# Kernel tuning notes

Measured on AMD Instinct MI355X. Metric: run time of the kernel, lower is better.

The kernel has to match this reference:

```python
import jax, jax.numpy as jnp
import numpy as np

DIM = 1024
HEADS = 16
DIM_HEAD = 64
INNER = HEADS * DIM_HEAD  # 1024
MAX_POS = 512
B, N = 2, 1024


def setup_inputs() -> dict:
    key = jax.random.key(0)
    ks = jax.random.split(key, 6)
    s = DIM ** -0.5
    x = jax.random.normal(ks[0], (B, N, DIM), dtype=jnp.float32)
    Wq = jax.random.normal(ks[1], (DIM, INNER), dtype=jnp.float32) * s
    Wkv = jax.random.normal(ks[2], (DIM, 2 * INNER), dtype=jnp.float32) * s
    Wo = jax.random.normal(ks[3], (INNER, DIM), dtype=jnp.float32) * (INNER ** -0.5)
    bo = jnp.zeros((DIM,), dtype=jnp.float32)
    rel_emb = jax.random.normal(ks[4], (2 * MAX_POS + 1, DIM_HEAD), dtype=jnp.float32)
    return {"x": x, "Wq": Wq, "Wkv": Wkv, "Wo": Wo, "bo": bo, "rel_emb": rel_emb}


def reference(x, Wq, Wkv, Wo, bo, rel_emb):
    b, n, _ = x.shape
    scale = DIM_HEAD ** -0.5
    q = x @ Wq                    # [b, n, inner]
    kv = x @ Wkv                  # [b, n, 2*inner]
    k, v = jnp.split(kv, 2, axis=-1)

    def split_heads(t):
        return t.reshape(b, n, HEADS, DIM_HEAD).transpose(0, 2, 1, 3)  # [b,h,n,d]

    q, k, v = map(split_heads, (q, k, v))
    dots = jnp.einsum('bhid,bhjd->bhij', q, k) * scale

    seq = jnp.arange(n)
    dist = jnp.clip(seq[:, None] - seq[None, :], -MAX_POS, MAX_POS) + MAX_POS  # [n, n]
    rel = rel_emb[dist]           # [n, n, d]
    pos_attn = jnp.einsum('bhnd,nrd->bhnr', q, rel) * scale
    dots = dots + pos_attn

    attn = jax.nn.softmax(dots, axis=-1)
    out = jnp.einsum('bhij,bhjd->bhid', attn, v)
    out = out.transpose(0, 2, 1, 3).reshape(b, n, INNER)
    return out @ Wo + bo
```

## Files before the change

### kernel.cpp

```cpp
#include <hip/hip_runtime.h>

typedef __bf16 bf16x8 __attribute__((ext_vector_type(8)));
typedef float f32x4 __attribute__((ext_vector_type(4)));

#define DEV __device__ __forceinline__

DEV unsigned short f2bf(float f) {
  union { float f; unsigned u; } x; x.f = f;
  unsigned r = x.u + 0x7FFFu + ((x.u >> 16) & 1u);
  return (unsigned short)(r >> 16);
}
DEV float bf2f(unsigned short h) {
  union { unsigned u; float f; } x; x.u = ((unsigned)h) << 16;
  return x.f;
}
DEV unsigned short bfc(float f) {
  union { __bf16 b; unsigned short u; } c; c.b = (__bf16)f; return c.u;
}

typedef __attribute__((address_space(3))) void* lds_vp;
typedef const __attribute__((address_space(1))) void* gbl_vp;
DEV void load_lds16(const unsigned short* gp, void* lp) {
  __builtin_amdgcn_global_load_lds((gbl_vp)(const void*)gp, (lds_vp)lp, 16, 0, 0);
}

__global__ __launch_bounds__(256)
void prep_k(const float* __restrict__ x, const float* __restrict__ rel,
            const float* __restrict__ bo, const float* __restrict__ Wq,
            const float* __restrict__ Wkv, const float* __restrict__ Wo,
            unsigned short* __restrict__ xb, unsigned short* __restrict__ relb,
            unsigned short* __restrict__ bob, unsigned short* __restrict__ WqkvT,
            unsigned short* __restrict__ WoT) {
  __shared__ unsigned short tile[32][33];
  const int bid = blockIdx.x, tid = threadIdx.x;
  if (bid < 2114) {
    const float* src; unsigned short* dst; long base; long n;
    if (bid < 2048)      { src = x;   dst = xb;   base = (long)bid * 1024;          n = 2097152; }
    else if (bid < 2113) { src = rel; dst = relb; base = (long)(bid - 2048) * 1024; n = 65600; }
    else                 { src = bo;  dst = bob;  base = 0;                          n = 1024; }
    long i = base + tid * 4;
    if (i < n) {
      float4 v = *(const float4*)&src[i];
      unsigned long long u = (unsigned long long)f2bf(v.x)
                           | ((unsigned long long)f2bf(v.y) << 16)
                           | ((unsigned long long)f2bf(v.z) << 32)
                           | ((unsigned long long)f2bf(v.w) << 48);
      *(unsigned long long*)&dst[i] = u;
    }
  } else {
    int id = bid - 2114;
    const float* src; unsigned short* dst; const int R = 1024; int C, txt, tyt;
    if (id < 1024)      { src = Wq;  dst = WqkvT;           C = 1024; txt = id & 31; tyt = id >> 5; }
    else if (id < 3072) { int l = id - 1024; src = Wkv; dst = WqkvT + 1048576; C = 2048; txt = l & 63; tyt = l >> 6; }
    else                { int l = id - 3072; src = Wo;  dst = WoT;             C = 1024; txt = l & 31; tyt = l >> 5; }
    int c0 = txt * 32, r0 = tyt * 32;
    int tx = tid & 31, ty = tid >> 5;
    #pragma unroll
    for (int i = 0; i < 4; ++i)
      tile[ty + i * 8][tx] = f2bf(src[(size_t)(r0 + ty + i * 8) * C + c0 + tx]);
    __syncthreads();
    #pragma unroll
    for (int i = 0; i < 4; ++i)
      dst[(size_t)(c0 + ty + i * 8) * R + r0 + tx] = tile[tx][ty + i * 8];
  }
}

DEV void stage16(const unsigned short* gbase, size_t gstride,
                 unsigned short* lbase, int r0, int lane) {
  #pragma unroll
  for (int t = 0; t < 2; ++t) {
    int r = r0 + t * 8 + (lane >> 3);
    int lc = (lane & 7) ^ (r & 7);
    load_lds16(&gbase[(size_t)r * gstride + lc * 8], &lbase[(size_t)(r0 + t * 8) * 64]);
  }
}
DEV bf16x8 read_swz(const unsigned short* buf, int row, int lc) {
  int pc = lc ^ (row & 7);
  return *(const bf16x8*)&buf[row * 64 + pc * 8];
}

__global__ __launch_bounds__(256)
void gemm_qkv(const unsigned short* __restrict__ A,
              const unsigned short* __restrict__ Bt,
              unsigned short* __restrict__ o0,
              unsigned short* __restrict__ o1,
              unsigned short* __restrict__ o2) {
  __shared__ __align__(16) unsigned short As[64 * 64];
  __shared__ __align__(16) unsigned short Bs[128 * 64];
  __shared__ unsigned short tbuf[64][68];
  const int tid  = threadIdx.x;
  const int lane = tid & 63, wave = tid >> 6;
  const int q15  = lane & 15, quad = lane >> 4;
  const int wr = wave >> 1, wc = wave & 1;
  const int m0 = blockIdx.y * 64, n0 = blockIdx.x * 128;
  const int K = 1024;

  f32x4 acc[2][4] = {};
  for (int k0 = 0; k0 < K; k0 += 64) {
    __syncthreads();
    stage16(&A[(size_t)m0 * K + k0], K, As, wave * 16, lane);
    stage16(&Bt[(size_t)n0 * K + k0], K, Bs, wave * 32, lane);
    stage16(&Bt[(size_t)n0 * K + k0], K, Bs, wave * 32 + 16, lane);
    __syncthreads();
    #pragma unroll
    for (int ks = 0; ks < 2; ++ks) {
      bf16x8 af[2], bfr[4];
      #pragma unroll
      for (int i = 0; i < 2; ++i)
        af[i] = read_swz(As, wr * 32 + i * 16 + q15, ks * 4 + quad);
      #pragma unroll
      for (int j = 0; j < 4; ++j)
        bfr[j] = read_swz(Bs, wc * 64 + j * 16 + q15, ks * 4 + quad);
      #pragma unroll
      for (int i = 0; i < 2; ++i)
        #pragma unroll
        for (int j = 0; j < 4; ++j)
          acc[i][j] = __builtin_amdgcn_mfma_f32_16x16x32_bf16(af[i], bfr[j], acc[i][j], 0, 0, 0);
    }
  }

  const int b = m0 >> 10, nn0 = m0 & 1023;
  if (n0 < 2048) {
    #pragma unroll
    for (int i = 0; i < 2; ++i)
      #pragma unroll
      for (int j = 0; j < 4; ++j)
        #pragma unroll
        for (int r = 0; r < 4; ++r) {
          int row = m0 + wr * 32 + i * 16 + quad * 4 + r;
          int col = n0 + wc * 64 + j * 16 + q15;
          float v = acc[i][j][r];
          int nn = row & 1023;
          unsigned short* dst; int c = col; float sc = 1.f;
          if (col < 1024) { dst = o0; sc = 0.125f; }
          else            { dst = o1; c = col - 1024; }
          int h = c >> 6, dd = c & 63;
          dst[((size_t)((row >> 10) * 16 + h) * 1024 + nn) * 64 + dd] = f2bf(v * sc);
        }
  } else {
    const int hp = (n0 - 2048) >> 6;
    #pragma unroll
    for (int hh = 0; hh < 2; ++hh) {
      __syncthreads();
      if (wc == hh) {
        #pragma unroll
        for (int i = 0; i < 2; ++i)
          #pragma unroll
          for (int j = 0; j < 4; ++j)
            #pragma unroll
            for (int r = 0; r < 4; ++r)
              tbuf[wr * 32 + i * 16 + quad * 4 + r][j * 16 + q15] = f2bf(acc[i][j][r]);
      }
      __syncthreads();
      const int bh = b * 16 + hp + hh;
      const int d = tid >> 2, nb = (tid & 3) * 16;
      #pragma unroll
      for (int s = 0; s < 2; ++s) {
        int n = nb + s * 8;
        union { uint4 v; unsigned short us[8]; } t;
        #pragma unroll
        for (int e = 0; e < 8; ++e) t.us[e] = tbuf[n + e][d];
        *(uint4*)&o2[((size_t)bh * 64 + d) * 1024 + nn0 + n] = t.v;
      }
    }
  }
}

__global__ __launch_bounds__(256)
void flash_attn(const unsigned short* __restrict__ q_ws,
                const unsigned short* __restrict__ k_ws,
                const unsigned short* __restrict__ vt_ws,
                const unsigned short* __restrict__ rel,
                unsigned short* __restrict__ ao) {
  __shared__ __align__(16) unsigned short Kbuf[2][64 * 64];
  __shared__ __align__(16) unsigned short Vbuf[2][64 * 64];
  __shared__ __align__(16) unsigned short P_lds[4][16 * 64];
  __shared__ __align__(16) unsigned short T_lds[4][16][84];

  const int tid  = threadIdx.x;
  const int lane = tid & 63, w = tid >> 6;
  const int q15  = lane & 15, quad = lane >> 4;
  const int bh = blockIdx.x;
  const int ib = blockIdx.y * 64 + w * 16;

  const unsigned short* qp = q_ws  + (size_t)bh * 1024 * 64;
  const unsigned short* kp = k_ws  + (size_t)bh * 1024 * 64;
  const unsigned short* tp = vt_ws + (size_t)bh * 64 * 1024;

  unsigned short* Trow = &T_lds[w][q15][0];
  unsigned short* Prow = &P_lds[w][q15 * 64];

  bf16x8 aq[2];
  #pragma unroll
  for (int ks = 0; ks < 2; ++ks)
    aq[ks] = *(const bf16x8*)&qp[(size_t)(ib + q15) * 64 + ks * 32 + quad * 8];

  f32x4 o[4] = {};
  float l_acc = 0.f;

  stage16(kp, 64, &Kbuf[0][0], w * 16, lane);
  stage16(tp, 1024, &Vbuf[0][0], w * 16, lane);
  bf16x8 rr[2][5];
  {
    const int tb = ib + 512 - 63;
    #pragma unroll
    for (int ks = 0; ks < 2; ++ks)
      #pragma unroll
      for (int ub = 0; ub < 5; ++ub) {
        int trow = tb + ub * 16 + q15;
        trow = trow < 0 ? 0 : (trow > 1024 ? 1024 : trow);
        rr[ks][ub] = *(const bf16x8*)&rel[(size_t)trow * 64 + ks * 32 + quad * 8];
      }
  }

  for (int jt = 0; jt < 16; ++jt) {
    const int j0 = jt * 64, cur = jt & 1;
    __builtin_amdgcn_s_barrier();
    if (jt + 1 < 16) {
      stage16(kp + (size_t)(j0 + 64) * 64, 64, &Kbuf[cur ^ 1][0], w * 16, lane);
      stage16(tp + (j0 + 64), 1024, &Vbuf[cur ^ 1][0], w * 16, lane);
    }

    f32x4 accT[5] = {};
    #pragma unroll
    for (int ks = 0; ks < 2; ++ks)
      #pragma unroll
      for (int ub = 0; ub < 5; ++ub)
        accT[ub] = __builtin_amdgcn_mfma_f32_16x16x32_bf16(rr[ks][ub], aq[ks], accT[ub], 0, 0, 0);
    #pragma unroll
    for (int ub = 0; ub < 5; ++ub) {
      uint2 tw;
      tw.x = (unsigned)bfc(accT[ub][0]) | ((unsigned)bfc(accT[ub][1]) << 16);
      tw.y = (unsigned)bfc(accT[ub][2]) | ((unsigned)bfc(accT[ub][3]) << 16);
      *(uint2*)&Trow[ub * 16 + quad * 4] = tw;
    }

    if (jt + 1 < 16) {
      const int tb = ib - (j0 + 64) + 512 - 63;
      #pragma unroll
      for (int ks = 0; ks < 2; ++ks)
        #pragma unroll
        for (int ub = 0; ub < 5; ++ub) {
          int trow = tb + ub * 16 + q15;
          trow = trow < 0 ? 0 : (trow > 1024 ? 1024 : trow);
          rr[ks][ub] = *(const bf16x8*)&rel[(size_t)trow * 64 + ks * 32 + quad * 8];
        }
    }

    __builtin_amdgcn_sched_barrier(0);

    f32x4 accS[4] = {};
    #pragma unroll
    for (int ks = 0; ks < 2; ++ks)
      #pragma unroll
      for (int cb = 0; cb < 4; ++cb) {
        bf16x8 bk = read_swz(&Kbuf[cur][0], cb * 16 + q15, ks * 4 + quad);
        accS[cb] = __builtin_amdgcn_mfma_f32_16x16x32_bf16(bk, aq[ks], accS[cb], 0, 0, 0);
      }

    #pragma unroll
    for (int cb = 0; cb < 4; ++cb) {
      float p[4];
      #pragma unroll
      for (int r = 0; r < 4; ++r) {
        int jl = cb * 16 + quad * 4 + r;
        float s = accS[cb][r] + bf2f(Trow[63 + q15 - jl]);
        p[r] = exp2f(fmaf(s, 1.44269504f, -64.f));
        l_acc += p[r];
      }
      uint2 pw;
      pw.x = (unsigned)bfc(p[0]) | ((unsigned)bfc(p[1]) << 16);
      pw.y = (unsigned)bfc(p[2]) | ((unsigned)bfc(p[3]) << 16);
      int phys = (cb * 2 + (quad >> 1)) ^ (q15 & 7);
      *(uint2*)&Prow[phys * 8 + (quad & 1) * 4] = pw;
    }

    #pragma unroll
    for (int ks = 0; ks < 2; ++ks) {
      bf16x8 ap = *(const bf16x8*)&Prow[(((ks * 4 + quad) ^ (q15 & 7))) * 8];
      #pragma unroll
      for (int db = 0; db < 4; ++db) {
        bf16x8 bv = read_swz(&Vbuf[cur][0], db * 16 + q15, ks * 4 + quad);
        o[db] = __builtin_amdgcn_mfma_f32_16x16x32_bf16(bv, ap, o[db], 0, 0, 0);
      }
    }
  }

  l_acc += __shfl_xor(l_acc, 16, 64);
  l_acc += __shfl_xor(l_acc, 32, 64);
  float inv = 1.f / (l_acc + 1e-30f);

  unsigned short* Bt = &T_lds[w][0][0];
  #pragma unroll
  for (int db = 0; db < 4; ++db) {
    uint2 bw;
    bw.x = (unsigned)bfc(o[db][0] * inv) | ((unsigned)bfc(o[db][1] * inv) << 16);
    bw.y = (unsigned)bfc(o[db][2] * inv) | ((unsigned)bfc(o[db][3] * inv) << 16);
    *(uint2*)&Bt[q15 * 72 + db * 16 + quad * 4] = bw;
  }
  const int il = lane >> 2, ch = (lane & 3) * 16;
  bf16x8 u0 = *(const bf16x8*)&Bt[il * 72 + ch];
  bf16x8 u1 = *(const bf16x8*)&Bt[il * 72 + ch + 8];
  const int b = bh >> 4, h = bh & 15;
  size_t addr = ((size_t)(b * 1024 + blockIdx.y * 64 + w * 16 + il)) * 1024
              + h * 64 + ch;
  *(bf16x8*)&ao[addr] = u0;
  *(bf16x8*)&ao[addr + 8] = u1;
}

__global__ __launch_bounds__(256)
void gemm_out(const unsigned short* __restrict__ A,
              const unsigned short* __restrict__ Bt,
              const unsigned short* __restrict__ bias,
              float* __restrict__ fo) {
  __shared__ __align__(16) unsigned short As[64 * 64];
  __shared__ __align__(16) unsigned short Bs[64 * 64];
  const int tid  = threadIdx.x;
  const int lane = tid & 63, w = tid >> 6;
  const int q15  = lane & 15, quad = lane >> 4;
  const int m0 = blockIdx.y * 64, n0 = blockIdx.x * 64;
  const int K = 1024, N = 1024;

  f32x4 acc[4] = {};
  for (int k0 = 0; k0 < K; k0 += 64) {
    __syncthreads();
    stage16(&A[(size_t)m0 * K + k0], K, As, w * 16, lane);
    stage16(&Bt[(size_t)n0 * K + k0], K, Bs, w * 16, lane);
    __syncthreads();
    #pragma unroll
    for (int ks = 0; ks < 2; ++ks) {
      bf16x8 af = read_swz(As, w * 16 + q15, ks * 4 + quad);
      bf16x8 bfr[4];
      #pragma unroll
      for (int j = 0; j < 4; ++j)
        bfr[j] = read_swz(Bs, j * 16 + q15, ks * 4 + quad);
      #pragma unroll
      for (int j = 0; j < 4; ++j)
        acc[j] = __builtin_amdgcn_mfma_f32_16x16x32_bf16(af, bfr[j], acc[j], 0, 0, 0);
    }
  }
  #pragma unroll
  for (int j = 0; j < 4; ++j)
    #pragma unroll
    for (int r = 0; r < 4; ++r) {
      int row = m0 + w * 16 + quad * 4 + r;
      int col = n0 + j * 16 + q15;
      fo[(size_t)row * N + col] = acc[j][r] + bf2f(bias[col]);
    }
}

extern "C" void kernel_launch(void* const* d_in, const int* in_sizes, int n_in,
                              void* d_out, int out_size, void* d_ws, size_t ws_size,
                              hipStream_t stream) {
  (void)in_sizes; (void)n_in; (void)out_size; (void)ws_size;
  const float* x   = (const float*)d_in[0];
  const float* Wq  = (const float*)d_in[1];
  const float* Wkv = (const float*)d_in[2];
  const float* Wo  = (const float*)d_in[3];
  const float* bo  = (const float*)d_in[4];
  const float* rel = (const float*)d_in[5];
  float* out = (float*)d_out;

  unsigned short* ws = (unsigned short*)d_ws;
  unsigned short* WoT   = ws;
  unsigned short* relb  = WoT   + 1048576;
  unsigned short* bob   = relb  + 65664;
  unsigned short* q_ws  = bob   + 1088;
  unsigned short* k_ws  = q_ws  + 2097152;
  unsigned short* vT    = k_ws  + 2097152;
  unsigned short* WqkvT = vT    + 2097152;
  unsigned short* xb    = WqkvT + 3145728;
  unsigned short* ao    = WqkvT;

  prep_k<<<6210, 256, 0, stream>>>(x, rel, bo, Wq, Wkv, Wo,
                                   xb, relb, bob, WqkvT, WoT);
  gemm_qkv<<<dim3(24, 32), 256, 0, stream>>>(xb, WqkvT, q_ws, k_ws, vT);
  flash_attn<<<dim3(32, 16), 256, 0, stream>>>(q_ws, k_ws, vT, relb, ao);
  gemm_out<<<dim3(16, 32), 256, 0, stream>>>(ao, WoT, bob, out);
}
```

Measured before the change: 161.0 us.

## Software-pipeline flash attention: compute next tile's scores during current softmax/PV

Restructures the attention loop into a one-tile-ahead software pipeline. The QK^T scores and relative-position T tile for tile p+1 are computed while tile p's softmax and PV MFMAs run. To support this it triple-buffers V, double-buffers T, and prefetches K/V two tiles ahead, with an explicit vmcnt wait before the barrier. It also sets launch_bounds to 2 blocks per SIMD occupancy. The aim is to overlap MFMA, exp and memory latency, at the cost of more LDS and register pressure and a fragile hand-tuned wait count.

```diff
diff --git a/kernel.cpp b/kernel.cpp
--- a/kernel.cpp
+++ b/kernel.cpp
@@ -166,16 +166,55 @@
   }
 }
 
-__global__ __launch_bounds__(256)
+DEV void load_rel(bf16x8 rr[2][5], const unsigned short* rel, int ib, int t,
+                  int q15, int quad) {
+  const int tb = ib - t * 64 + 512 - 63;
+  #pragma unroll
+  for (int ks = 0; ks < 2; ++ks)
+    #pragma unroll
+    for (int ub = 0; ub < 5; ++ub) {
+      int trow = tb + ub * 16 + q15;
+      trow = trow < 0 ? 0 : (trow > 1024 ? 1024 : trow);
+      rr[ks][ub] = *(const bf16x8*)&rel[(size_t)trow * 64 + ks * 32 + quad * 8];
+    }
+}
+DEV void t_phase(const bf16x8 rr[2][5], const bf16x8 aq[2],
+                 unsigned short* Tw, int quad) {
+  f32x4 accT[5] = {};
+  #pragma unroll
+  for (int ks = 0; ks < 2; ++ks)
+    #pragma unroll
+    for (int ub = 0; ub < 5; ++ub)
+      accT[ub] = __builtin_amdgcn_mfma_f32_16x16x32_bf16(rr[ks][ub], aq[ks], accT[ub], 0, 0, 0);
+  #pragma unroll
+  for (int ub = 0; ub < 5; ++ub) {
+    uint2 tw;
+    tw.x = (unsigned)bfc(accT[ub][0]) | ((unsigned)bfc(accT[ub][1]) << 16);
+    tw.y = (unsigned)bfc(accT[ub][2]) | ((unsigned)bfc(accT[ub][3]) << 16);
+    *(uint2*)&Tw[ub * 16 + quad * 4] = tw;
+  }
+}
+DEV void s_phase(f32x4 acc[4], const unsigned short* Kb, const bf16x8 aq[2],
+                 int q15, int quad) {
+  #pragma unroll
+  for (int ks = 0; ks < 2; ++ks)
+    #pragma unroll
+    for (int cb = 0; cb < 4; ++cb) {
+      bf16x8 bk = read_swz(Kb, cb * 16 + q15, ks * 4 + quad);
+      acc[cb] = __builtin_amdgcn_mfma_f32_16x16x32_bf16(bk, aq[ks], acc[cb], 0, 0, 0);
+    }
+}
+
+__global__ __launch_bounds__(256, 2)
 void flash_attn(const unsigned short* __restrict__ q_ws,
                 const unsigned short* __restrict__ k_ws,
                 const unsigned short* __restrict__ vt_ws,
                 const unsigned short* __restrict__ rel,
                 unsigned short* __restrict__ ao) {
   __shared__ __align__(16) unsigned short Kbuf[2][64 * 64];
-  __shared__ __align__(16) unsigned short Vbuf[2][64 * 64];
+  __shared__ __align__(16) unsigned short Vbuf[3][64 * 64];
   __shared__ __align__(16) unsigned short P_lds[4][16 * 64];
-  __shared__ __align__(16) unsigned short T_lds[4][16][84];
+  __shared__ __align__(16) unsigned short T_lds[2][4][16][84];
 
   const int tid  = threadIdx.x;
   const int lane = tid & 63, w = tid >> 6;
@@ -187,7 +226,8 @@
   const unsigned short* kp = k_ws  + (size_t)bh * 1024 * 64;
   const unsigned short* tp = vt_ws + (size_t)bh * 64 * 1024;
 
-  unsigned short* Trow = &T_lds[w][q15][0];
+  unsigned short* T0 = &T_lds[0][w][q15][0];
+  unsigned short* T1 = &T_lds[1][w][q15][0];
   unsigned short* Prow = &P_lds[w][q15 * 64];
 
   bf16x8 aq[2];
@@ -201,76 +241,47 @@
   stage16(kp, 64, &Kbuf[0][0], w * 16, lane);
   stage16(tp, 1024, &Vbuf[0][0], w * 16, lane);
   bf16x8 rr[2][5];
-  {
-    const int tb = ib + 512 - 63;
-    #pragma unroll
-    for (int ks = 0; ks < 2; ++ks)
-      #pragma unroll
-      for (int ub = 0; ub < 5; ++ub) {
-        int trow = tb + ub * 16 + q15;
-        trow = trow < 0 ? 0 : (trow > 1024 ? 1024 : trow);
-        rr[ks][ub] = *(const bf16x8*)&rel[(size_t)trow * 64 + ks * 32 + quad * 8];
-      }
-  }
-
-  for (int jt = 0; jt < 16; ++jt) {
-    const int j0 = jt * 64, cur = jt & 1;
-    __builtin_amdgcn_s_barrier();
-    if (jt + 1 < 16) {
-      stage16(kp + (size_t)(j0 + 64) * 64, 64, &Kbuf[cur ^ 1][0], w * 16, lane);
-      stage16(tp + (j0 + 64), 1024, &Vbuf[cur ^ 1][0], w * 16, lane);
-    }
-
-    f32x4 accT[5] = {};
-    #pragma unroll
-    for (int ks = 0; ks < 2; ++ks)
-      #pragma unroll
-      for (int ub = 0; ub < 5; ++ub)
-        accT[ub] = __builtin_amdgcn_mfma_f32_16x16x32_bf16(rr[ks][ub], aq[ks], accT[ub], 0, 0, 0);
-    #pragma unroll
-    for (int ub = 0; ub < 5; ++ub) {
-      uint2 tw;
-      tw.x = (unsigned)bfc(accT[ub][0]) | ((unsigned)bfc(accT[ub][1]) << 16);
-      tw.y = (unsigned)bfc(accT[ub][2]) | ((unsigned)bfc(accT[ub][3]) << 16);
-      *(uint2*)&Trow[ub * 16 + quad * 4] = tw;
-    }
-
-    if (jt + 1 < 16) {
-      const int tb = ib - (j0 + 64) + 512 - 63;
-      #pragma unroll
-      for (int ks = 0; ks < 2; ++ks)
-        #pragma unroll
-        for (int ub = 0; ub < 5; ++ub) {
-          int trow = tb + ub * 16 + q15;
-          trow = trow < 0 ? 0 : (trow > 1024 ? 1024 : trow);
-          rr[ks][ub] = *(const bf16x8*)&rel[(size_t)trow * 64 + ks * 32 + quad * 8];
-        }
-    }
-
+  load_rel(rr, rel, ib, 0, q15, quad);
+  stage16(kp + (size_t)64 * 64, 64, &Kbuf[1][0], w * 16, lane);
+  stage16(tp + 64, 1024, &Vbuf[1][0], w * 16, lane);
+  t_phase(rr, aq, T0, quad);
+  load_rel(rr, rel, ib, 1, q15, quad);
+  __syncthreads();
+  f32x4 sc_[4] = {};
+  s_phase(sc_, &Kbuf[0][0], aq, q15, quad);
+  __builtin_amdgcn_sched_barrier(0);
+  __syncthreads();
+
+  for (int p = 0; p < 16; ++p) {
+    const int vr = p % 3, vs = (p + 2) % 3;
+    if (p < 14) {
+      stage16(kp + (size_t)(p + 2) * 64 * 64, 64, &Kbuf[p & 1][0], w * 16, lane);
+      stage16(tp + (p + 2) * 64, 1024, &Vbuf[vs][0], w * 16, lane);
+    }
+    if (p < 15)
+      t_phase(rr, aq, (p & 1) ? T0 : T1, quad);
+    if (p < 14)
+      load_rel(rr, rel, ib, p + 2, q15, quad);
     __builtin_amdgcn_sched_barrier(0);
 
-    f32x4 accS[4] = {};
-    #pragma unroll
-    for (int ks = 0; ks < 2; ++ks)
-      #pragma unroll
-      for (int cb = 0; cb < 4; ++cb) {
-        bf16x8 bk = read_swz(&Kbuf[cur][0], cb * 16 + q15, ks * 4 + quad);
-        accS[cb] = __builtin_amdgcn_mfma_f32_16x16x32_bf16(bk, aq[ks], accS[cb], 0, 0, 0);
-      }
-
+    f32x4 sn_[4] = {};
+    if (p < 15)
+      s_phase(sn_, &Kbuf[(p + 1) & 1][0], aq, q15, quad);
+
+    const unsigned short* Tr = (p & 1) ? T1 : T0;
     #pragma unroll
     for (int cb = 0; cb < 4; ++cb) {
-      float p[4];
+      float pv[4];
       #pragma unroll
       for (int r = 0; r < 4; ++r) {
         int jl = cb * 16 + quad * 4 + r;
-        float s = accS[cb][r] + bf2f(Trow[63 + q15 - jl]);
-        p[r] = exp2f(fmaf(s, 1.44269504f, -64.f));
-        l_acc += p[r];
+        float s = sc_[cb][r] + bf2f(Tr[63 + q15 - jl]);
+        pv[r] = exp2f(fmaf(s, 1.44269504f, -64.f));
+        l_acc += pv[r];
       }
       uint2 pw;
-      pw.x = (unsigned)bfc(p[0]) | ((unsigned)bfc(p[1]) << 16);
-      pw.y = (unsigned)bfc(p[2]) | ((unsigned)bfc(p[3]) << 16);
+      pw.x = (unsigned)bfc(pv[0]) | ((unsigned)bfc(pv[1]) << 16);
+      pw.y = (unsigned)bfc(pv[2]) | ((unsigned)bfc(pv[3]) << 16);
       int phys = (cb * 2 + (quad >> 1)) ^ (q15 & 7);
       *(uint2*)&Prow[phys * 8 + (quad & 1) * 4] = pw;
     }
@@ -280,17 +291,24 @@
       bf16x8 ap = *(const bf16x8*)&Prow[(((ks * 4 + quad) ^ (q15 & 7))) * 8];
       #pragma unroll
       for (int db = 0; db < 4; ++db) {
-        bf16x8 bv = read_swz(&Vbuf[cur][0], db * 16 + q15, ks * 4 + quad);
+        bf16x8 bv = read_swz(&Vbuf[vr][0], db * 16 + q15, ks * 4 + quad);
         o[db] = __builtin_amdgcn_mfma_f32_16x16x32_bf16(bv, ap, o[db], 0, 0, 0);
       }
     }
+
+    #pragma unroll
+    for (int cb = 0; cb < 4; ++cb) sc_[cb] = sn_[cb];
+
+    __builtin_amdgcn_sched_barrier(0);
+    asm volatile("s_waitcnt vmcnt(10)" ::: "memory");
+    __builtin_amdgcn_s_barrier();
   }
 
   l_acc += __shfl_xor(l_acc, 16, 64);
   l_acc += __shfl_xor(l_acc, 32, 64);
   float inv = 1.f / (l_acc + 1e-30f);
 
-  unsigned short* Bt = &T_lds[w][0][0];
+  unsigned short* Bt = &T_lds[0][w][0][0];
   #pragma unroll
   for (int db = 0; db < 4; ++db) {
     uint2 bw;
```

Result: no change. 161.9 us (+0.6%).
